# Performance work log

Hardware: AMD Instinct MI355X
Metric: run time of the kernel (lower is better)

Reference implementation:

```python
import jax, jax.numpy as jnp
import numpy as np

D_MODEL = 1024
NUM_HEADS = 16
DEPTH = D_MODEL // NUM_HEADS


def setup_inputs() -> dict:
    key = jax.random.key(0)
    k_x, k_wqkv, k_bqkv, k_wp, k_bp = jax.random.split(key, 5)
    B, N = 2, 2048
    x = jax.random.normal(k_x, (B, N, D_MODEL), dtype=jnp.float32)
    scale = 1.0 / np.sqrt(D_MODEL)
    Wqkv = jax.random.normal(k_wqkv, (D_MODEL, 3 * D_MODEL), dtype=jnp.float32) * scale
    bqkv = jnp.zeros((3 * D_MODEL,), dtype=jnp.float32)
    Wproj = jax.random.normal(k_wp, (D_MODEL, D_MODEL), dtype=jnp.float32) * scale
    bproj = jnp.zeros((D_MODEL,), dtype=jnp.float32)
    return {"x": x, "Wqkv": Wqkv, "bqkv": bqkv, "Wproj": Wproj, "bproj": bproj}


def reference(x, Wqkv, bqkv, Wproj, bproj):
    B, N, C = x.shape
    # QKV projection; original layout: [B, N, H, depth, 3] -> transpose to [B, 3, H, N, depth]
    qkv = x @ Wqkv + bqkv                      # [B, N, 3C]
    qkv = qkv.reshape(B, N, NUM_HEADS, DEPTH, 3)
    qkv = jnp.transpose(qkv, (0, 4, 2, 1, 3))  # [B, 3, H, N, depth]
    q, k, v = qkv[:, 0], qkv[:, 1], qkv[:, 2]  # each [B, H, N, depth]
    # scaled dot-product attention (full N x N scores, as in the original)
    scale = 1.0 / jnp.sqrt(jnp.asarray(DEPTH, dtype=x.dtype))
    attn = jnp.einsum("bhnd,bhmd->bhnm", q, k) * scale
    attn = jax.nn.softmax(attn.astype(jnp.float32), axis=-1).astype(x.dtype)
    out = jnp.einsum("bhnm,bhmd->bhnd", attn, v)  # [B, H, N, depth]
    out = jnp.transpose(out, (0, 2, 1, 3)).reshape(B, N, C)
    return out @ Wproj + bproj
```

## Files before the change

kernel.cpp:

```cpp
#include <hip/hip_runtime.h>
#include <stdint.h>

#define D_MODEL 1024
#define NHEADS  16
#define DEPTH   64
#define BATCH   2
#define SEQ     2048
#define M_TOK   (BATCH*SEQ)

typedef __attribute__((ext_vector_type(8)))  short short8;
typedef __attribute__((ext_vector_type(4)))  float f32x4;
typedef __attribute__((ext_vector_type(16))) float f32x16;
typedef __attribute__((ext_vector_type(4)))  unsigned int uint4v;

#if defined(__has_builtin)
#if __has_builtin(__builtin_amdgcn_exp2f)
#define EXP2(x) __builtin_amdgcn_exp2f(x)
#endif
#endif
#ifndef EXP2
#define EXP2(x) exp2f(x)
#endif

__device__ __forceinline__ unsigned short f2bf(float f) {
  unsigned int u = __float_as_uint(f);
  u += 0x7fffu + ((u >> 16) & 1u);
  return (unsigned short)(u >> 16);
}

__device__ __forceinline__ unsigned int cvt_pk_bf16(float lo, float hi) {
  unsigned int r;
  asm("v_cvt_pk_bf16_f32 %0, %1, %2" : "=v"(r) : "v"(lo), "v"(hi));
  return r;
}

__device__ __forceinline__ void gload_lds16(const unsigned short* g, unsigned short* l) {
  __builtin_amdgcn_global_load_lds((const __attribute__((address_space(1))) void*)g,
                                   (__attribute__((address_space(3))) void*)l, 16, 0, 0);
}

__global__ void mha_prep(const float* __restrict__ x, const float* __restrict__ Wqkv,
                         const float* __restrict__ Wproj,
                         unsigned short* __restrict__ xb,
                         unsigned short* __restrict__ wqkT,
                         unsigned short* __restrict__ wvT,
                         unsigned short* __restrict__ wpT) {
  __shared__ float tile[32][33];
  int id = blockIdx.x, t = threadIdx.x;
  if (id < 2048) {
    int i = (id * 256 + t) * 8;
    float4 a = *(const float4*)(x + i);
    float4 b = *(const float4*)(x + i + 4);
    uint4 r;
    r.x = (unsigned)f2bf(a.x) | ((unsigned)f2bf(a.y) << 16);
    r.y = (unsigned)f2bf(a.z) | ((unsigned)f2bf(a.w) << 16);
    r.z = (unsigned)f2bf(b.x) | ((unsigned)f2bf(b.y) << 16);
    r.w = (unsigned)f2bf(b.z) | ((unsigned)f2bf(b.w) << 16);
    *(uint4*)(xb + i) = r;
  } else if (id < 5120) {
    int b = id - 2048;
    int c0 = (b % 96) * 32, k0 = (b / 96) * 32;
    int tx = t & 31, ty = t >> 5;
    for (int i = ty; i < 32; i += 8)
      tile[i][tx] = Wqkv[(size_t)(k0 + i) * 3072 + c0 + tx];
    __syncthreads();
    for (int i = ty; i < 32; i += 8) {
      int c = c0 + i;
      int hd = c / 3;
      int s = c - hd * 3;
      unsigned short v = f2bf(tile[tx][i]);
      if (s < 2) wqkT[(size_t)(s * 1024 + hd) * 1024 + k0 + tx] = v;
      else       wvT [(size_t)hd * 1024 + k0 + tx] = v;
    }
  } else {
    int b = id - 5120;
    int c0 = (b & 31) * 32, k0 = (b >> 5) * 32;
    int tx = t & 31, ty = t >> 5;
    for (int i = ty; i < 32; i += 8)
      tile[i][tx] = Wproj[(size_t)(k0 + i) * 1024 + c0 + tx];
    __syncthreads();
    for (int i = ty; i < 32; i += 8)
      wpT[(size_t)(c0 + i) * 1024 + k0 + tx] = f2bf(tile[tx][i]);
  }
}

__global__ __launch_bounds__(256, 3) void mha_gemm_qkv(
    const unsigned short* __restrict__ xb,
    const unsigned short* __restrict__ wqkT,
    const unsigned short* __restrict__ wvT,
    const float* __restrict__ bias,
    unsigned short* __restrict__ Qb,
    unsigned short* __restrict__ Kb,
    unsigned short* __restrict__ Vtb)
{
  __shared__ __align__(16) unsigned short As[128 * 32];
  __shared__ __align__(16) unsigned short Bs[128 * 32];
  const int K = 1024;
  int id = blockIdx.x;
  bool m0 = id < 512;
  int bx, by, bz = 0;
  const unsigned short *A, *Bt;
  if (m0) { bx = id & 15; by = id >> 4; A = xb; Bt = wqkT; }
  else {
    int b2 = id - 512;
    bx = b2 & 15; by = (b2 >> 4) & 7; bz = b2 >> 7;
    A = wvT; Bt = xb + (size_t)bz * SEQ * D_MODEL;
  }
  int t = threadIdx.x;
  int wv = t >> 6, lane = t & 63;
  int l15 = lane & 15, l4 = lane >> 4;
  int wr = wv >> 1, wc = wv & 1;
  int blkM = by * 128, blkN = bx * 128;

  f32x4 acc[4][4];
  for (int m = 0; m < 4; m++) for (int n = 0; n < 4; n++) acc[m][n] = (f32x4){0.f,0.f,0.f,0.f};

  int srow = t >> 2;
  int skc  = (t & 3) * 8;
  for (int kt = 0; kt < K; kt += 32) {
    #pragma unroll
    for (int i = 0; i < 2; i++) {
      int e = i * 256 + t;
      int row = srow + i * 64;
      gload_lds16(A  + (size_t)(blkM + row) * K + kt + skc, As + e * 8);
      gload_lds16(Bt + (size_t)(blkN + row) * K + kt + skc, Bs + e * 8);
    }
    __syncthreads();
    short8 af[4], bf[4];
    #pragma unroll
    for (int m = 0; m < 4; m++)
      af[m] = *(const short8*)&As[(wr * 64 + m * 16 + l15) * 32 + l4 * 8];
    #pragma unroll
    for (int n = 0; n < 4; n++)
      bf[n] = *(const short8*)&Bs[(wc * 64 + n * 16 + l15) * 32 + l4 * 8];
    #pragma unroll
    for (int m = 0; m < 4; m++)
      #pragma unroll
      for (int n = 0; n < 4; n++)
        acc[m][n] = __builtin_amdgcn_mfma_f32_16x16x32_bf16(af[m], bf[n], acc[m][n], 0, 0, 0);
    __syncthreads();
  }

  int row0 = blkM + wr * 64;
  int col0 = blkN + wc * 64;
  #pragma unroll
  for (int m = 0; m < 4; m++) {
    #pragma unroll
    for (int n = 0; n < 4; n++) {
      int colb = col0 + n * 16 + l15;
      #pragma unroll
      for (int j = 0; j < 4; j++) {
        int row = row0 + m * 16 + l4 * 4 + j;
        float v = acc[m][n][j];
        if (m0) {
          int s = colb >> 10, hd = colb & 1023;
          v += bias[hd * 3 + s];
          if (s == 0) v *= 0.18033688011112042f;
          size_t idx = ((size_t)((row >> 11) * NHEADS + (hd >> 6)) * SEQ + (row & 2047)) * DEPTH + (hd & 63);
          (s == 0 ? Qb : Kb)[idx] = f2bf(v);
        } else {
          v += bias[row * 3 + 2];
          Vtb[((size_t)(bz * 1024 + row)) * SEQ + colb] = f2bf(v);
        }
      }
    }
  }
}

__global__ __launch_bounds__(256, 3) void mha_gemm_proj(
    const unsigned short* __restrict__ A,
    const unsigned short* __restrict__ Bt,
    const float* __restrict__ bias,
    float* __restrict__ out_f)
{
  __shared__ __align__(16) unsigned short As[128 * 32];
  __shared__ __align__(16) unsigned short Bs[64 * 32];
  const int K = 1024;
  int t = threadIdx.x;
  int wv = t >> 6, lane = t & 63;
  int l15 = lane & 15, l4 = lane >> 4;
  int wr = wv >> 1, wc = wv & 1;
  int blkM = blockIdx.y * 128, blkN = blockIdx.x * 64;

  f32x4 acc[4][2];
  for (int m = 0; m < 4; m++) for (int n = 0; n < 2; n++) acc[m][n] = (f32x4){0.f,0.f,0.f,0.f};

  int srow = t >> 2;
  int skc  = (t & 3) * 8;
  for (int kt = 0; kt < K; kt += 32) {
    #pragma unroll
    for (int i = 0; i < 2; i++) {
      int row = srow + i * 64;
      gload_lds16(A + (size_t)(blkM + row) * K + kt + skc, As + (i * 256 + t) * 8);
    }
    gload_lds16(Bt + (size_t)(blkN + srow) * K + kt + skc, Bs + t * 8);
    __syncthreads();
    short8 af[4], bf[2];
    #pragma unroll
    for (int m = 0; m < 4; m++)
      af[m] = *(const short8*)&As[(wr * 64 + m * 16 + l15) * 32 + l4 * 8];
    #pragma unroll
    for (int n = 0; n < 2; n++)
      bf[n] = *(const short8*)&Bs[(wc * 32 + n * 16 + l15) * 32 + l4 * 8];
    #pragma unroll
    for (int m = 0; m < 4; m++)
      #pragma unroll
      for (int n = 0; n < 2; n++)
        acc[m][n] = __builtin_amdgcn_mfma_f32_16x16x32_bf16(af[m], bf[n], acc[m][n], 0, 0, 0);
    __syncthreads();
  }

  int row0 = blkM + wr * 64;
  int col0 = blkN + wc * 32;
  #pragma unroll
  for (int m = 0; m < 4; m++) {
    #pragma unroll
    for (int n = 0; n < 2; n++) {
      int colb = col0 + n * 16 + l15;
      #pragma unroll
      for (int j = 0; j < 4; j++) {
        int row = row0 + m * 16 + l4 * 4 + j;
        out_f[(size_t)row * D_MODEL + colb] = acc[m][n][j] + bias[colb];
      }
    }
  }
}

__global__ __launch_bounds__(512, 2) void mha_attn(
    const unsigned short* __restrict__ Q,
    const unsigned short* __restrict__ Kb,
    const unsigned short* __restrict__ Vt,
    unsigned short* __restrict__ O)
{
  const int N = SEQ;
  const int NIT = N / 64;
  int id = blockIdx.x;
  int bh    = (id & 7) * 4 + ((id >> 7) & 3);
  int qtile = (id >> 3) & 15;
  int t = threadIdx.x, wv = t >> 6, lane = t & 63;
  int l31 = lane & 31, hi = lane >> 5;
  int kh = wv & 1, qh = wv >> 1;

  __shared__ __align__(16) unsigned short SMEM[2 * 8192];
  __shared__ float CMB[4][64][33];

  const unsigned short* Kbh = Kb + (size_t)bh * N * DEPTH;
  const unsigned short* Vbh = Vt + (size_t)bh * DEPTH * N;

  int qrow = qtile * 128 + qh * 32 + l31;
  const unsigned short* Qp = Q + ((size_t)bh * N + qrow) * DEPTH + hi * 8;
  short8 qf[4];
  #pragma unroll
  for (int c = 0; c < 4; c++) qf[c] = *(const short8*)(Qp + c * 16);

  int srow = t >> 3;
  int sc8  = ((t & 7) ^ (srow & 7)) * 8;
  const unsigned short* kst = Kbh + (size_t)srow * DEPTH + sc8;
  const unsigned short* vst = Vbh + (size_t)srow * N + sc8;

  int rbK = (kh * 32 + l31) * 64;
  int rbV0 = l31 * 64, rbV1 = rbV0 + 2048;
  int goQK[4], goPV[2];
  #pragma unroll
  for (int c = 0; c < 4; c++) goQK[c] = ((c * 2 + hi) ^ (l31 & 7)) * 8;
  #pragma unroll
  for (int lc = 0; lc < 2; lc++) goPV[lc] = ((kh * 4 + lc * 2 + hi) ^ (l31 & 7)) * 8;

  short8 ones;
  #pragma unroll
  for (int i = 0; i < 8; i++) ones[i] = (short)0x3F80;

  f32x16 o0, o1, lsacc, zc;
  #pragma unroll
  for (int i = 0; i < 16; i++) { o0[i] = 0.f; o1[i] = 0.f; lsacc[i] = 0.f; zc[i] = 0.f; }

  gload_lds16(kst, SMEM + t * 8);
  gload_lds16(vst, SMEM + 4096 + t * 8);
  asm volatile("s_waitcnt vmcnt(0)" ::: "memory");
  __builtin_amdgcn_sched_barrier(0);
  __builtin_amdgcn_s_barrier();
  __builtin_amdgcn_sched_barrier(0);

#define BODY(BUF, IT)                                                                   \
  do {                                                                                  \
    if ((IT) + 1 < NIT) {                                                               \
      gload_lds16(kst + (size_t)((IT) + 1) * 4096, SMEM + ((BUF) ^ 1) * 8192 + t * 8);  \
      gload_lds16(vst + ((IT) + 1) * 64, SMEM + ((BUF) ^ 1) * 8192 + 4096 + t * 8);     \
    }                                                                                   \
    {                                                                                   \
      const unsigned short* Kc = SMEM + (BUF) * 8192;                                   \
      const unsigned short* Vc = Kc + 4096;                                             \
      __builtin_amdgcn_s_setprio(1);                                                    \
      short8 ka0 = *(const short8*)&Kc[rbK + goQK[0]];                                  \
      f32x16 s = __builtin_amdgcn_mfma_f32_32x32x16_bf16(ka0, qf[0], zc, 0, 0, 0);      \
      _Pragma("unroll") for (int c = 1; c < 4; c++) {                                   \
        short8 ka = *(const short8*)&Kc[rbK + goQK[c]];                                 \
        s = __builtin_amdgcn_mfma_f32_32x32x16_bf16(ka, qf[c], s, 0, 0, 0);             \
      }                                                                                 \
      __builtin_amdgcn_s_setprio(0);                                                    \
      float p[16];                                                                      \
      _Pragma("unroll") for (int r = 0; r < 16; r++) p[r] = EXP2(s[r]);                 \
      _Pragma("unroll") for (int lc = 0; lc < 2; lc++) {                                \
        unsigned int X0 = cvt_pk_bf16(p[8*lc+0], p[8*lc+1]);                            \
        unsigned int X1 = cvt_pk_bf16(p[8*lc+2], p[8*lc+3]);                            \
        unsigned int X2 = cvt_pk_bf16(p[8*lc+4], p[8*lc+5]);                            \
        unsigned int X3 = cvt_pk_bf16(p[8*lc+6], p[8*lc+7]);                            \
        auto r02 = __builtin_amdgcn_permlane32_swap(X0, X2, false, false);              \
        auto r13 = __builtin_amdgcn_permlane32_swap(X1, X3, false, false);              \
        uint4v wvec; wvec[0] = r02[0]; wvec[1] = r13[0]; wvec[2] = r02[1]; wvec[3] = r13[1]; \
        short8 bfrag = __builtin_bit_cast(short8, wvec);                                \
        short8 va = *(const short8*)&Vc[rbV0 + goPV[lc]];                               \
        short8 vb = *(const short8*)&Vc[rbV1 + goPV[lc]];                               \
        __builtin_amdgcn_s_setprio(1);                                                  \
        o0 = __builtin_amdgcn_mfma_f32_32x32x16_bf16(va, bfrag, o0, 0, 0, 0);           \
        o1 = __builtin_amdgcn_mfma_f32_32x32x16_bf16(vb, bfrag, o1, 0, 0, 0);           \
        lsacc = __builtin_amdgcn_mfma_f32_32x32x16_bf16(ones, bfrag, lsacc, 0, 0, 0);   \
        __builtin_amdgcn_s_setprio(0);                                                  \
      }                                                                                 \
    }                                                                                   \
    if ((IT) + 1 < NIT) {                                                               \
      asm volatile("s_waitcnt vmcnt(0)" ::: "memory");                                  \
      __builtin_amdgcn_sched_barrier(0);                                                \
      __builtin_amdgcn_s_barrier();                                                     \
      __builtin_amdgcn_sched_barrier(0);                                                \
    }                                                                                   \
  } while (0)

  for (int it2 = 0; it2 < NIT; it2 += 2) {
    BODY(0, it2);
    BODY(1, it2 + 1);
  }
#undef BODY

  float ls = lsacc[0];

  if (kh == 1) {
    float* c0 = &CMB[qh][lane][0];
    #pragma unroll
    for (int i = 0; i < 16; i++) { c0[i] = o0[i]; c0[16 + i] = o1[i]; }
    c0[32] = ls;
  }
  __syncthreads();
  if (kh == 0) {
    const float* c0 = &CMB[qh][lane][0];
    #pragma unroll
    for (int i = 0; i < 16; i++) { o0[i] += c0[i]; o1[i] += c0[16 + i]; }
    float rl = 1.0f / (ls + c0[32]);

    int b = bh >> 4, h = bh & 15;
    unsigned short* Op = O + ((size_t)b * N + qrow) * D_MODEL + h * DEPTH;
    #pragma unroll
    for (int gq = 0; gq < 4; gq++) {
      #pragma unroll
      for (int rp = 0; rp < 2; rp++) {
        int reg = gq * 4 + rp * 2;
        int d = gq * 8 + hi * 4 + rp * 2;
        *(unsigned int*)(Op + d)      = cvt_pk_bf16(o0[reg] * rl, o0[reg + 1] * rl);
        *(unsigned int*)(Op + 32 + d) = cvt_pk_bf16(o1[reg] * rl, o1[reg + 1] * rl);
      }
    }
  }
}

extern "C" void kernel_launch(void* const* d_in, const int* in_sizes, int n_in,
                              void* d_out, int out_size, void* d_ws, size_t ws_size,
                              hipStream_t stream) {
  const float* x     = (const float*)d_in[0];
  const float* Wqkv  = (const float*)d_in[1];
  const float* bqkv  = (const float*)d_in[2];
  const float* Wproj = (const float*)d_in[3];
  const float* bproj = (const float*)d_in[4];
  float* out = (float*)d_out;

  char* w = (char*)d_ws;
  unsigned short* xb    = (unsigned short*)(w);
  unsigned short* wqkT  = (unsigned short*)(w + 8388608);
  unsigned short* wvT   = (unsigned short*)(w + 8388608 + 4194304);
  unsigned short* wpT   = (unsigned short*)(w + 8388608 + 4194304 + 2097152);
  unsigned short* Qbuf  = (unsigned short*)(w + 16777216);
  unsigned short* Kbuf  = (unsigned short*)(w + 16777216 + 8388608);
  unsigned short* Vtb   = (unsigned short*)(w + 16777216 + 16777216);
  unsigned short* AOut  = (unsigned short*)(w + 16777216 + 25165824);

  mha_prep<<<6144, 256, 0, stream>>>(x, Wqkv, Wproj, xb, wqkT, wvT, wpT);
  mha_gemm_qkv<<<768, 256, 0, stream>>>(xb, wqkT, wvT, bqkv, Qbuf, Kbuf, Vtb);
  mha_attn<<<512, 512, 0, stream>>>(Qbuf, Kbuf, Vtb, AOut);
  mha_gemm_proj<<<dim3(16, 32), 256, 0, stream>>>(AOut, wpT, bproj, out);
}
```

Baseline: 119.8 us.

## Double GEMM K-tile, XOR-swizzle LDS, and remap blocks per XCD

New measurement: 111.3 us. 7.1% less time.

```diff
diff --git a/kernel.cpp b/kernel.cpp
--- a/kernel.cpp
+++ b/kernel.cpp
@@ -93,15 +93,19 @@
     unsigned short* __restrict__ Kb,
     unsigned short* __restrict__ Vtb)
 {
-  __shared__ __align__(16) unsigned short As[128 * 32];
-  __shared__ __align__(16) unsigned short Bs[128 * 32];
+  __shared__ __align__(16) unsigned short As[128 * 64];
+  __shared__ __align__(16) unsigned short Bs[128 * 64];
   const int K = 1024;
   int id = blockIdx.x;
   bool m0 = id < 512;
   int bx, by, bz = 0;
   const unsigned short *A, *Bt;
-  if (m0) { bx = id & 15; by = id >> 4; A = xb; Bt = wqkT; }
-  else {
+  if (m0) {
+    int xcd = id & 7, idx = id >> 3;
+    by = xcd * 4 + (idx >> 4);
+    bx = idx & 15;
+    A = xb; Bt = wqkT;
+  } else {
     int b2 = id - 512;
     bx = b2 & 15; by = (b2 >> 4) & 7; bz = b2 >> 7;
     A = wvT; Bt = xb + (size_t)bz * SEQ * D_MODEL;
@@ -115,29 +119,32 @@
   f32x4 acc[4][4];
   for (int m = 0; m < 4; m++) for (int n = 0; n < 4; n++) acc[m][n] = (f32x4){0.f,0.f,0.f,0.f};
 
-  int srow = t >> 2;
-  int skc  = (t & 3) * 8;
-  for (int kt = 0; kt < K; kt += 32) {
-    #pragma unroll
-    for (int i = 0; i < 2; i++) {
+  for (int kt = 0; kt < K; kt += 64) {
+    #pragma unroll
+    for (int i = 0; i < 4; i++) {
       int e = i * 256 + t;
-      int row = srow + i * 64;
-      gload_lds16(A  + (size_t)(blkM + row) * K + kt + skc, As + e * 8);
-      gload_lds16(Bt + (size_t)(blkN + row) * K + kt + skc, Bs + e * 8);
-    }
-    __syncthreads();
-    short8 af[4], bf[4];
-    #pragma unroll
-    for (int m = 0; m < 4; m++)
-      af[m] = *(const short8*)&As[(wr * 64 + m * 16 + l15) * 32 + l4 * 8];
-    #pragma unroll
-    for (int n = 0; n < 4; n++)
-      bf[n] = *(const short8*)&Bs[(wc * 64 + n * 16 + l15) * 32 + l4 * 8];
-    #pragma unroll
-    for (int m = 0; m < 4; m++)
+      int row = e >> 3;
+      int sc = ((e & 7) ^ (row & 7)) * 8;
+      gload_lds16(A  + (size_t)(blkM + row) * K + kt + sc, As + e * 8);
+      gload_lds16(Bt + (size_t)(blkN + row) * K + kt + sc, Bs + e * 8);
+    }
+    __syncthreads();
+    #pragma unroll
+    for (int kk = 0; kk < 2; kk++) {
+      int gp = ((kk * 4 + l4) ^ (l15 & 7)) * 8;
+      short8 af[4], bf[4];
+      #pragma unroll
+      for (int m = 0; m < 4; m++)
+        af[m] = *(const short8*)&As[(wr * 64 + m * 16 + l15) * 64 + gp];
       #pragma unroll
       for (int n = 0; n < 4; n++)
-        acc[m][n] = __builtin_amdgcn_mfma_f32_16x16x32_bf16(af[m], bf[n], acc[m][n], 0, 0, 0);
+        bf[n] = *(const short8*)&Bs[(wc * 64 + n * 16 + l15) * 64 + gp];
+      #pragma unroll
+      for (int m = 0; m < 4; m++)
+        #pragma unroll
+        for (int n = 0; n < 4; n++)
+          acc[m][n] = __builtin_amdgcn_mfma_f32_16x16x32_bf16(af[m], bf[n], acc[m][n], 0, 0, 0);
+    }
     __syncthreads();
   }
 
@@ -173,40 +180,54 @@
     const float* __restrict__ bias,
     float* __restrict__ out_f)
 {
-  __shared__ __align__(16) unsigned short As[128 * 32];
-  __shared__ __align__(16) unsigned short Bs[64 * 32];
+  __shared__ __align__(16) unsigned short As[128 * 64];
+  __shared__ __align__(16) unsigned short Bs[64 * 64];
   const int K = 1024;
+  int id = blockIdx.x;
+  int xcd = id & 7, idx = id >> 3;
+  int by = xcd * 4 + (idx >> 4);
+  int bx = idx & 15;
   int t = threadIdx.x;
   int wv = t >> 6, lane = t & 63;
   int l15 = lane & 15, l4 = lane >> 4;
   int wr = wv >> 1, wc = wv & 1;
-  int blkM = blockIdx.y * 128, blkN = blockIdx.x * 64;
+  int blkM = by * 128, blkN = bx * 64;
 
   f32x4 acc[4][2];
   for (int m = 0; m < 4; m++) for (int n = 0; n < 2; n++) acc[m][n] = (f32x4){0.f,0.f,0.f,0.f};
 
-  int srow = t >> 2;
-  int skc  = (t & 3) * 8;
-  for (int kt = 0; kt < K; kt += 32) {
+  for (int kt = 0; kt < K; kt += 64) {
+    #pragma unroll
+    for (int i = 0; i < 4; i++) {
+      int e = i * 256 + t;
+      int row = e >> 3;
+      int sc = ((e & 7) ^ (row & 7)) * 8;
+      gload_lds16(A + (size_t)(blkM + row) * K + kt + sc, As + e * 8);
+    }
     #pragma unroll
     for (int i = 0; i < 2; i++) {
-      int row = srow + i * 64;
-      gload_lds16(A + (size_t)(blkM + row) * K + kt + skc, As + (i * 256 + t) * 8);
-    }
-    gload_lds16(Bt + (size_t)(blkN + srow) * K + kt + skc, Bs + t * 8);
-    __syncthreads();
-    short8 af[4], bf[2];
-    #pragma unroll
-    for (int m = 0; m < 4; m++)
-      af[m] = *(const short8*)&As[(wr * 64 + m * 16 + l15) * 32 + l4 * 8];
-    #pragma unroll
-    for (int n = 0; n < 2; n++)
-      bf[n] = *(const short8*)&Bs[(wc * 32 + n * 16 + l15) * 32 + l4 * 8];
-    #pragma unroll
-    for (int m = 0; m < 4; m++)
+      int e = i * 256 + t;
+      int row = e >> 3;
+      int sc = ((e & 7) ^ (row & 7)) * 8;
+      gload_lds16(Bt + (size_t)(blkN + row) * K + kt + sc, Bs + e * 8);
+    }
+    __syncthreads();
+    #pragma unroll
+    for (int kk = 0; kk < 2; kk++) {
+      int gp = ((kk * 4 + l4) ^ (l15 & 7)) * 8;
+      short8 af[4], bf[2];
+      #pragma unroll
+      for (int m = 0; m < 4; m++)
+        af[m] = *(const short8*)&As[(wr * 64 + m * 16 + l15) * 64 + gp];
       #pragma unroll
       for (int n = 0; n < 2; n++)
-        acc[m][n] = __builtin_amdgcn_mfma_f32_16x16x32_bf16(af[m], bf[n], acc[m][n], 0, 0, 0);
+        bf[n] = *(const short8*)&Bs[(wc * 32 + n * 16 + l15) * 64 + gp];
+      #pragma unroll
+      for (int m = 0; m < 4; m++)
+        #pragma unroll
+        for (int n = 0; n < 2; n++)
+          acc[m][n] = __builtin_amdgcn_mfma_f32_16x16x32_bf16(af[m], bf[n], acc[m][n], 0, 0, 0);
+    }
     __syncthreads();
   }
 
@@ -385,5 +406,5 @@
   mha_prep<<<6144, 256, 0, stream>>>(x, Wqkv, Wproj, xb, wqkT, wvT, wpT);
   mha_gemm_qkv<<<768, 256, 0, stream>>>(xb, wqkT, wvT, bqkv, Qbuf, Kbuf, Vtb);
   mha_attn<<<512, 512, 0, stream>>>(Qbuf, Kbuf, Vtb, AOut);
-  mha_gemm_proj<<<dim3(16, 32), 256, 0, stream>>>(AOut, wpT, bproj, out);
-}
+  mha_gemm_proj<<<512, 256, 0, stream>>>(AOut, wpT, bproj, out);
+}
```
